# Kernel tuning notes

Measured on AMD Instinct MI355X. Metric: run time of the kernel, lower is better.

Reference implementation:

```python
import jax, jax.numpy as jnp
import numpy as np
import math

E, NNODE = 32768, 2048          # edges, nodes
NUM_SPECIES, EMB = 100, 32
MUL, HIDDEN, N_RBF, LMAX, ENV_P = 16, 256, 8, 3, 6
SL = {0: slice(0, 1), 1: slice(1, 4), 2: slice(4, 9), 3: slice(9, 16)}  # SH blocks


def _cg(j1, m1, j2, m2, j3, m3):
    """Clebsch-Gordan coefficient (Racah formula), complex SH basis."""
    if m1 + m2 != m3:
        return 0.0
    f = math.factorial
    pre = math.sqrt((2*j3+1) * f(j1+j2-j3) * f(j1-j2+j3) * f(-j1+j2+j3) / f(j1+j2+j3+1))
    pre *= math.sqrt(f(j3+m3)*f(j3-m3)*f(j1-m1)*f(j1+m1)*f(j2-m2)*f(j2+m2))
    s = 0.0
    kmin = max(0, j2 - j3 - m1, j1 - j3 + m2)
    kmax = min(j1 + j2 - j3, j1 - m1, j2 + m2)
    for k in range(kmin, kmax + 1):
        s += (-1)**k / (f(k)*f(j1+j2-j3-k)*f(j1-m1-k)*f(j2+m2-k)*f(j3-j2+m1+k)*f(j3-j1-m2+k))
    return pre * s


def _umat(l):
    """Complex->real spherical-harmonics change of basis."""
    U = np.zeros((2*l+1, 2*l+1), dtype=complex)
    U[l, l] = 1.0
    s2 = 1.0 / math.sqrt(2.0)
    for m in range(1, l + 1):
        U[l+m, l-m] = s2
        U[l+m, l+m] = (-1)**m * s2
        U[l-m, l-m] = 1j * s2
        U[l-m, l+m] = -1j * (-1)**m * s2
    return U


def _real_coupling(l1, l2, l3):
    """Real-basis CG coupling tensor, Frobenius-normalized (w3j analogue)."""
    C = np.zeros((2*l1+1, 2*l2+1, 2*l3+1), dtype=complex)
    for a, m1 in enumerate(range(-l1, l1+1)):
        for b, m2 in enumerate(range(-l2, l2+1)):
            for c, m3 in enumerate(range(-l3, l3+1)):
                C[a, b, c] = _cg(l1, m1, l2, m2, l3, m3)
    T = np.einsum('am,bn,ck,mnk->abc', _umat(l1), _umat(l2), _umat(l3).conj(), C)
    Tr, Ti = np.real(T), np.imag(T)
    T = Tr if np.linalg.norm(Tr) >= np.linalg.norm(Ti) else Ti
    n = np.linalg.norm(T)
    return None if n < 1e-8 else (T / n).astype(np.float32)


PATHS = {l3: [] for l3 in range(LMAX + 1)}
for _l1 in range(LMAX + 1):
    for _l2 in range(LMAX + 1):
        for _l3 in range(abs(_l1 - _l2), min(_l1 + _l2, LMAX) + 1):
            _T = _real_coupling(_l1, _l2, _l3)
            if _T is not None:
                PATHS[_l3].append((_l1, _l2, jnp.asarray(_T)))
NPATH = {l3: len(PATHS[l3]) for l3 in range(LMAX + 1)}


def envelope(d):  # polynomial smoothing envelope, p=6, cutoff=1
    p = ENV_P
    e = 1.0 - 0.5*(p+1)*(p+2)*d**p + p*(p+2)*d**(p+1) - 0.5*p*(p+1)*d**(p+2)
    return jnp.where(d < 1.0, e, 0.0)


def bessel(d):  # radial Bessel basis [E] -> [E, N_RBF]
    n = jnp.arange(1, N_RBF + 1, dtype=d.dtype)
    ds = jnp.where(d == 0.0, 1.0, d)[:, None]
    return (math.sqrt(2.0) * jnp.sin(n * jnp.pi * ds) / ds) * envelope(d)[:, None]


def sph_harm16(u):  # real SH l=0..3, component norm (|Y_l|^2 = 2l+1), [E,16]
    x, y, z = u[:, 0], u[:, 1], u[:, 2]
    x2, y2, z2 = x*x, y*y, z*z
    s3, s15, s5 = math.sqrt(3.0), math.sqrt(15.0), math.sqrt(5.0)
    s358, s105 = math.sqrt(35.0/8.0), math.sqrt(105.0)
    s218, s7 = math.sqrt(21.0/8.0), math.sqrt(7.0)
    return jnp.stack([
        jnp.ones_like(x),
        s3*y, s3*z, s3*x,
        s15*x*y, s15*y*z, 0.5*s5*(3*z2 - 1), s15*x*z, 0.5*s15*(x2 - y2),
        s358*y*(3*x2 - y2), s105*x*y*z, s218*y*(5*z2 - 1), 0.5*s7*(5*z2 - 3)*z,
        s218*x*(5*z2 - 1), 0.5*s105*(x2 - y2)*z, s358*x*(x2 - y2),
    ], axis=1)


def dense(x, W):  # e3nn-style bias-free linear, 1/sqrt(fan_in)
    return (x @ W) / math.sqrt(W.shape[0])


def dense_axis(V, W):  # [E,C,K] x [C,D] -> [E,D,K]
    return jnp.einsum('eck,cd->edk', V, W) / math.sqrt(W.shape[0])


def tensor_product(A, B, lmax_out):
    """CG tensor product [E,MUL,16] x [E,MUL,16] -> {l3: [E,MUL*npath,2l3+1]}."""
    out = {}
    for l3 in range(lmax_out + 1):
        scale = math.sqrt(2*l3 + 1)
        parts = [scale * jnp.einsum('ijk,emi,emj->emk', T, A[:, :, SL[l1]], B[:, :, SL[l2]])
                 for (l1, l2, T) in PATHS[l3]]
        out[l3] = jnp.concatenate(parts, axis=1)
    return out


def allegro_layer(x, V, Y, senders, eps, env, alpha, Ww, Wl, Wv):
    w = dense(x, Ww)                                          # [E,MUL]
    node = jax.ops.segment_sum(w[:, :, None] * Y[:, None, :], senders, num_segments=NNODE)
    wY = node[senders] * eps                                  # scatter_sum + map_back
    lmax_out = LMAX if Wv is not None else 0
    tp = tensor_product(wY, V, lmax_out)
    xc = jnp.concatenate([x, tp[0][:, :, 0]], axis=1)         # fold 0e into scalars
    h = jax.nn.silu(dense(xc, Wl[0]))
    h = jax.nn.silu(dense(h, Wl[1]))
    y = env[:, None] * dense(h, Wl[2])
    a2 = alpha**2
    x = (x + a2 * y) / (1.0 + a2)
    if Wv is None:
        return x, None
    Vn = jnp.concatenate(
        [jnp.zeros((V.shape[0], MUL, 1), x.dtype)] +           # no 0e in output irreps
        [dense_axis(tp[l], Wv[l - 1]) for l in (1, 2, 3)], axis=2)
    return x, Vn


def _forward(vectors, varepsilon, alpha, emb, W_tb1, W_tb2, W_tb3, W_tb4,
             W_w0, W_w1, W_l11, W_l12, W_l13, W_v1, W_v2, W_v3,
             W_w2, W_l21, W_l22, W_l23, W_h, W_out,
             senders, receivers, species):
    d = jnp.linalg.norm(vectors, axis=1)
    u = vectors / jnp.where(d == 0.0, 1.0, d)[:, None]
    env = envelope(d)
    eps = 1.0 / jnp.sqrt(1.0 + varepsilon**2)
    x = jnp.concatenate([bessel(d), emb[species[senders]], emb[species[receivers]]], axis=1)
    x = jnp.where(d[:, None] == 0.0, 0.0, x)
    x = jax.nn.silu(dense(x, W_tb1))
    x = jax.nn.silu(dense(x, W_tb2))
    x = jax.nn.silu(dense(x, W_tb3))
    x = dense(x, W_tb4)
    x = env[:, None] * x                                      # [E,HIDDEN]
    Y = sph_harm16(u)                                         # [E,16]
    V = dense(x, W_w0)[:, :, None] * Y[:, None, :]            # [E,MUL,16]
    x, V = allegro_layer(x, V, Y, senders, eps, env, alpha,
                         W_w1, (W_l11, W_l12, W_l13), (W_v1, W_v2, W_v3))
    x, _ = allegro_layer(x, V, Y, senders, eps, env, alpha,
                         W_w2, (W_l21, W_l22, W_l23), None)
    x = dense(x, W_h)
    return env[:, None] * dense(x, W_out)                     # [E,1]


def setup_inputs():
    key = jax.random.key(0)
    ks = jax.random.split(key, 32)
    dirs = jax.random.normal(ks[0], (E, 3), dtype=jnp.float32)
    dirs = dirs / jnp.linalg.norm(dirs, axis=1, keepdims=True)
    r = jax.random.uniform(ks[1], (E, 1), minval=0.05, maxval=0.95, dtype=jnp.float32)
    w = lambda k, s: jax.random.normal(k, s, dtype=jnp.float32)
    n0 = NPATH[0]
    return {
        "vectors": dirs * r,
        "varepsilon": jnp.asarray(4.0, jnp.float32),   # sqrt(avg_num_neighbors=16)
        "alpha": jnp.asarray(1.0, jnp.float32),
        "emb": w(ks[5], (NUM_SPECIES, EMB)),
        "W_tb1": w(ks[6], (N_RBF + 2*EMB, HIDDEN // 8)),
        "W_tb2": w(ks[7], (HIDDEN // 8, HIDDEN // 4)),
        "W_tb3": w(ks[8], (HIDDEN // 4, HIDDEN // 2)),
        "W_tb4": w(ks[9], (HIDDEN // 2, HIDDEN)),
        "W_w0": w(ks[10], (HIDDEN, MUL)),
        "W_w1": w(ks[11], (HIDDEN, MUL)),
        "W_l11": w(ks[12], (HIDDEN + MUL * n0, HIDDEN)),
        "W_l12": w(ks[13], (HIDDEN, HIDDEN)),
        "W_l13": w(ks[14], (HIDDEN, HIDDEN)),
        "W_v1": w(ks[15], (MUL * NPATH[1], MUL)),
        "W_v2": w(ks[16], (MUL * NPATH[2], MUL)),
        "W_v3": w(ks[17], (MUL * NPATH[3], MUL)),
        "W_w2": w(ks[18], (HIDDEN, MUL)),
        "W_l21": w(ks[19], (HIDDEN + MUL * n0, HIDDEN)),
        "W_l22": w(ks[20], (HIDDEN, HIDDEN)),
        "W_l23": w(ks[21], (HIDDEN, HIDDEN)),
        "W_h": w(ks[22], (HIDDEN, 128)),
        "W_out": w(ks[23], (128, 1)),
        "senders": jax.random.randint(ks[2], (E,), 0, NNODE),
        "receivers": jax.random.randint(ks[3], (E,), 0, NNODE),
        "species": jax.random.randint(ks[4], (NNODE,), 0, NUM_SPECIES),
    }


def reference(vectors, varepsilon, alpha, emb, W_tb1, W_tb2, W_tb3, W_tb4,
              W_w0, W_w1, W_l11, W_l12, W_l13, W_v1, W_v2, W_v3,
              W_w2, W_l21, W_l22, W_l23, W_h, W_out,
              senders, receivers, species):
    return _forward(vectors, varepsilon, alpha, emb, W_tb1, W_tb2, W_tb3, W_tb4,
                    W_w0, W_w1, W_l11, W_l12, W_l13, W_v1, W_v2, W_v3,
                    W_w2, W_l21, W_l22, W_l23, W_h, W_out,
                    senders, receivers, species)
```

## Files before the change

kernel.cpp:

```cpp
#include <hip/hip_runtime.h>
#include <cmath>
#include <complex>
#include <cstdio>
#include <cstring>
#include <algorithm>

#define E_EDGES 32768
#define NNODES  2048
#define VN_E    128

namespace cgt {

static double fct(int n){
  static const double f[13] = {1.,1.,2.,6.,24.,120.,720.,5040.,40320.,362880.,
                               3628800.,39916800.,479001600.};
  return f[n];
}

static double cg(int j1,int m1,int j2,int m2,int j3,int m3){
  if (m1+m2 != m3) return 0.0;
  double pre = std::sqrt((2*j3+1)*fct(j1+j2-j3)*fct(j1-j2+j3)*fct(-j1+j2+j3)/fct(j1+j2+j3+1));
  pre *= std::sqrt(fct(j3+m3)*fct(j3-m3)*fct(j1-m1)*fct(j1+m1)*fct(j2-m2)*fct(j2+m2));
  int kmin = 0;
  if (j2-j3-m1 > kmin) kmin = j2-j3-m1;
  if (j1-j3+m2 > kmin) kmin = j1-j3+m2;
  int kmax = j1+j2-j3;
  if (j1-m1 < kmax) kmax = j1-m1;
  if (j2+m2 < kmax) kmax = j2+m2;
  double s = 0.0;
  for (int k=kmin;k<=kmax;k++){
    double d = fct(k)*fct(j1+j2-j3-k)*fct(j1-m1-k)*fct(j2+m2-k)*fct(j3-j2+m1+k)*fct(j3-j1-m2+k);
    s += ((k&1)? -1.0:1.0)/d;
  }
  return pre*s;
}

typedef std::complex<double> cd;

static void umat(int l, cd U[7][7]){
  for (int a=0;a<7;a++) for (int b=0;b<7;b++) U[a][b]=cd(0,0);
  U[l][l] = cd(1,0);
  double s2 = 1.0/std::sqrt(2.0);
  for (int m=1;m<=l;m++){
    double sg = (m&1)? -1.0 : 1.0;
    U[l+m][l-m] = cd(s2,0);
    U[l+m][l+m] = cd(sg*s2,0);
    U[l-m][l-m] = cd(0, s2);
    U[l-m][l+m] = cd(0, -sg*s2);
  }
}

static bool realCoupling(int l1,int l2,int l3, double T[7][7][7]){
  cd U1[7][7],U2[7][7],U3[7][7];
  umat(l1,U1); umat(l2,U2); umat(l3,U3);
  int n1=2*l1+1, n2=2*l2+1, n3=2*l3+1;
  double Cg[7][7][7];
  for (int m=0;m<n1;m++) for(int n=0;n<n2;n++) for(int k=0;k<n3;k++)
    Cg[m][n][k] = cg(l1,m-l1,l2,n-l2,l3,k-l3);
  double Tr[7][7][7], Ti[7][7][7];
  double nr=0, ni=0;
  for (int a=0;a<n1;a++) for(int b=0;b<n2;b++) for(int c=0;c<n3;c++){
    cd s(0,0);
    for (int m=0;m<n1;m++){
      if (U1[a][m]==cd(0,0)) continue;
      for (int n=0;n<n2;n++){
        if (U2[b][n]==cd(0,0)) continue;
        for (int k=0;k<n3;k++){
          double cgv = Cg[m][n][k];
          if (cgv==0.0) continue;
          s += U1[a][m]*U2[b][n]*std::conj(U3[c][k])*cgv;
        }
      }
    }
    Tr[a][b][c]=s.real(); Ti[a][b][c]=s.imag();
    nr += s.real()*s.real(); ni += s.imag()*s.imag();
  }
  bool useR = (nr >= ni);
  double nn = std::sqrt(useR? nr : ni);
  if (nn < 1e-8) return false;
  for (int a=0;a<n1;a++)for(int b=0;b<n2;b++)for(int c=0;c<n3;c++)
    T[a][b][c] = (useR? Tr[a][b][c] : Ti[a][b][c])/nn;
  return true;
}

struct Tables {
  float val[4096];
  int   ij[4096];
  int   pmeta[40*4];
  int   ccnt[40*8];
  int   l3base[4];
  int   l3np[4];
  int   npaths;
  int   nent;
  int   tptot;
  int   pairs[256];
  float TD[256*30*8];
  int   sl_origc[40];
  int   npairs;
};

struct PathTmp {
  int l1,l2,l3, tpoff, kd;
  int ec;
  double T[7][7][7];
};

static void build(Tables& tb){
  static PathTmp paths[40];
  int np = 0, tpoff = 0;
  int l3start[5];
  for (int l3=0;l3<=3;l3++){
    tb.l3base[l3] = tpoff;
    l3start[l3] = np;
    int kd = 2*l3+1;
    for (int l1=0;l1<=3;l1++) for (int l2=0;l2<=3;l2++){
      int lo = (l1>l2)? l1-l2 : l2-l1;
      int hi = std::min(l1+l2,3);
      if (l3 < lo || l3 > hi) continue;
      PathTmp& pt = paths[np];
      if (!realCoupling(l1,l2,l3,pt.T)) continue;
      pt.l1=l1; pt.l2=l2; pt.l3=l3; pt.kd=kd; pt.tpoff=tpoff;
      double scale = std::sqrt((double)kd);
      int cnt = 0;
      for (int a=0;a<2*l1+1;a++)for(int b=0;b<2*l2+1;b++)for(int c=0;c<kd;c++)
        if (std::fabs(pt.T[a][b][c]*scale) > 1e-7) cnt++;
      pt.ec = cnt;
      tpoff += 16*kd;
      np++;
    }
  }
  l3start[4] = np;
  for (int l3=0;l3<=3;l3++) tb.l3np[l3] = l3start[l3+1]-l3start[l3];
  static int order[40];
  for (int i=0;i<np;i++) order[i]=i;
  for (int l3=0;l3<=3;l3++)
    std::sort(order+l3start[l3], order+l3start[l3+1],
              [&](int a,int b){ return paths[a].ec > paths[b].ec; });
  std::memset(tb.TD, 0, sizeof(tb.TD));
  std::memset(tb.pairs, 0, sizeof(tb.pairs));
  static int pmap[16][16];
  for (int i=0;i<16;i++) for (int j=0;j<16;j++) pmap[i][j] = -1;
  int npr = 0;
  int ep = 0;
  for (int slot=0; slot<np; slot++){
    const PathTmp& pt = paths[order[slot]];
    double scale = std::sqrt((double)pt.kd);
    int s1 = pt.l1*pt.l1, s2 = pt.l2*pt.l2;
    tb.pmeta[slot*4+0] = pt.tpoff;
    tb.pmeta[slot*4+1] = ep;
    tb.sl_origc[slot] = ((pt.tpoff - tb.l3base[pt.l3]) / (16*pt.kd)) * 16;
    int tot = 0;
    for (int c=0;c<pt.kd;c++){
      int cnt = 0;
      for (int a=0;a<2*pt.l1+1;a++)for(int b=0;b<2*pt.l2+1;b++){
        double v = pt.T[a][b][c]*scale;
        if (std::fabs(v) > 1e-7){
          tb.val[ep] = (float)v;
          tb.ij[ep]  = (s1+a) | ((s2+b)<<8);
          ep++; cnt++;
          if (pt.l3 >= 1){
            int aa = s1+a, bb = s2+b;
            int pi = pmap[aa][bb];
            if (pi < 0){ pi = npr; pmap[aa][bb] = pi;
                         tb.pairs[npr] = aa | (bb<<8); npr++; }
            tb.TD[(pi*30 + (slot-4))*8 + c] = (float)v;
          }
        }
      }
      tb.ccnt[slot*8+c] = cnt;
      tot += cnt;
    }
    for (int c=pt.kd;c<8;c++) tb.ccnt[slot*8+c]=0;
    tb.pmeta[slot*4+2] = tot;
    tb.pmeta[slot*4+3] = pt.kd;
  }
  if (npr & 1){ tb.pairs[npr] = 0; npr++; }
  tb.npairs = npr;
  tb.npaths = np; tb.nent = ep; tb.tptot = tpoff;
}

}


enum GFlags { F_NONE=0, F_SILU=1, F_ENV=2, F_RESID=4 };

typedef _Float16 half8 __attribute__((ext_vector_type(8)));
typedef __attribute__((ext_vector_type(4))) float f32x4;

__device__ inline unsigned short f2h(float f){
  union { _Float16 h; unsigned short u; } x;
  x.h = (_Float16)f;
  return x.u;
}
__device__ inline float h2f(unsigned short u){
  union { _Float16 h; unsigned short u; } x; x.u = u;
  return (float)x.h;
}

__device__ inline int swz(int row, int kh){
  int b = row*64 + kh*2;
  return b ^ (((row >> 1) & 3) << 4);
}

template<int FLAGS, int A16>
__global__ __launch_bounds__(256) void mgemm_k(
    const void* __restrict__ A1v, const void* __restrict__ A2v,
    int K1, int K, const unsigned short* __restrict__ Wt, int N,
    unsigned short* Cout, const float* __restrict__ env,
    const float* __restrict__ alphap, const unsigned short* Xres)
{
  __shared__ unsigned short AsB[128*32];
  __shared__ unsigned short BsB[128*32];
  const int tid  = threadIdx.x;
  const int wave = tid >> 6, lane = tid & 63;
  const int bm = blockIdx.x*128, bn = blockIdx.y*128;
  const int wr = (wave >> 1)*64, wc = (wave & 1)*64;
  const int K2 = K - K1;
  f32x4 acc[4][4] = {};

  const int sr  = tid >> 3;
  const int skq = (tid & 7) * 4;
  const int sr2 = tid >> 1;
  const int skh = (tid & 1) * 16;
  const int bn_ = tid >> 1;
  const int bkh = (tid & 1) * 16;

  for (int k0 = 0; k0 < K; k0 += 32) {
    if (A16) {
      int kk = k0 + skh;
      const unsigned short* ap = (kk < K1)
        ? (const unsigned short*)A1v + (size_t)(bm + sr2)*K1 + kk
        : (const unsigned short*)A2v + (size_t)(bm + sr2)*K2 + (kk - K1);
      uint4 u0 = *(const uint4*)ap;
      uint4 u1 = *(const uint4*)(ap + 8);
      *(uint4*)((char*)AsB + swz(sr2, skh))     = u0;
      *(uint4*)((char*)AsB + swz(sr2, skh + 8)) = u1;
    } else {
#pragma unroll
      for (int q = 0; q < 4; q++) {
        int row = q*32 + sr;
        int grow = bm + row;
        int kk = k0 + skq;
        float4 f4 = (kk < K1)
          ? *(const float4*)((const float*)A1v + (size_t)grow*K1 + kk)
          : *(const float4*)((const float*)A2v + (size_t)grow*K2 + (kk - K1));
        ushort4 u;
        u.x = f2h(f4.x); u.y = f2h(f4.y); u.z = f2h(f4.z); u.w = f2h(f4.w);
        *(ushort4*)((char*)AsB + swz(row, skq)) = u;
      }
    }
    {
      const unsigned short* s = Wt + (size_t)(bn + bn_)*K + k0 + bkh;
#pragma unroll
      for (int q = 0; q < 4; q++) {
        ushort4 u = *(const ushort4*)(s + q*4);
        *(ushort4*)((char*)BsB + swz(bn_, bkh + q*4)) = u;
      }
    }
    __syncthreads();
    const int fr = lane & 15, fk = (lane >> 4) * 8;
    half8 af[4], bf[4];
#pragma unroll
    for (int i = 0; i < 4; i++)
      af[i] = *(half8*)((char*)AsB + swz(wr + i*16 + fr, fk));
#pragma unroll
    for (int j = 0; j < 4; j++)
      bf[j] = *(half8*)((char*)BsB + swz(wc + j*16 + fr, fk));
#pragma unroll
    for (int i = 0; i < 4; i++)
#pragma unroll
      for (int j = 0; j < 4; j++)
        acc[i][j] = __builtin_amdgcn_mfma_f32_16x16x32_f16(af[i], bf[j], acc[i][j], 0, 0, 0);
    __syncthreads();
  }

  const float rscale = 1.f/sqrtf((float)K);
  float a2 = 0.f, inv1a2 = 1.f;
  if (FLAGS & F_RESID) { float al = alphap[0]; a2 = al*al; inv1a2 = 1.f/(1.f+a2); }
#pragma unroll
  for (int i = 0; i < 4; i++) {
#pragma unroll
    for (int r = 0; r < 4; r++) {
      int row = bm + wr + i*16 + ((lane >> 4) << 2) + r;
      float ev = (FLAGS & F_ENV) ? env[row] : 1.f;
#pragma unroll
      for (int j = 0; j < 4; j++) {
        int col = bn + wc + j*16 + (lane & 15);
        float v = acc[i][j][r]*rscale;
        if (FLAGS & F_SILU) v = v/(1.f+__expf(-v));
        if (FLAGS & F_ENV)  v *= ev;
        if (FLAGS & F_RESID) v = (h2f(Xres[(size_t)row*N+col]) + a2*v)*inv1a2;
        Cout[(size_t)row*N+col] = f2h(v);
      }
    }
  }
}

__global__ __launch_bounds__(256) void mlp3_k(
    const unsigned short* __restrict__ X, const unsigned short* __restrict__ T0,
    const unsigned short* __restrict__ W1t, const unsigned short* __restrict__ W2t,
    const unsigned short* __restrict__ W3t, unsigned short* __restrict__ Out,
    const float* __restrict__ env, const float* __restrict__ alphap)
{
  __shared__ unsigned short AsB[64*32];
  __shared__ unsigned short BsB[256*32];
  __shared__ unsigned short Hs[64*264];
  const int tid  = threadIdx.x;
  const int wave = tid >> 6, lane = tid & 63;
  const int bm = blockIdx.x*64;
  const int wc = wave*64;
  const int fr = lane & 15, fk = (lane >> 4) * 8;
  const int r4 = (lane >> 4) << 2;
  const int sra = tid >> 2;
  const int ska = (tid & 3) * 8;
  const int srb = tid >> 1;
  const int skb = (tid & 1) * 16;
  f32x4 acc[4][4] = {};

  for (int k0 = 0; k0 < 320; k0 += 32) {
    {
      int kk = k0 + ska;
      const unsigned short* ap = (kk < 256)
        ? X  + (size_t)(bm + sra)*256 + kk
        : T0 + (size_t)(bm + sra)*64  + (kk - 256);
      uint4 u = *(const uint4*)ap;
      *(uint4*)((char*)AsB + swz(sra, ska)) = u;
    }
#pragma unroll
    for (int h = 0; h < 2; h++) {
      int n = h*128 + srb;
      const unsigned short* s = W1t + (size_t)n*320 + k0 + skb;
      uint4 u0 = *(const uint4*)s;
      uint4 u1 = *(const uint4*)(s + 8);
      *(uint4*)((char*)BsB + swz(n, skb))     = u0;
      *(uint4*)((char*)BsB + swz(n, skb + 8)) = u1;
    }
    __syncthreads();
    half8 af[4], bf[4];
#pragma unroll
    for (int i = 0; i < 4; i++)
      af[i] = *(half8*)((char*)AsB + swz(i*16 + fr, fk));
#pragma unroll
    for (int j = 0; j < 4; j++)
      bf[j] = *(half8*)((char*)BsB + swz(wc + j*16 + fr, fk));
#pragma unroll
    for (int i = 0; i < 4; i++)
#pragma unroll
      for (int j = 0; j < 4; j++)
        acc[i][j] = __builtin_amdgcn_mfma_f32_16x16x32_f16(af[i], bf[j], acc[i][j], 0, 0, 0);
    __syncthreads();
  }
  const float rs320 = 0.055901699437494740f;
#pragma unroll
  for (int i = 0; i < 4; i++)
#pragma unroll
    for (int r = 0; r < 4; r++) {
      int row = i*16 + r4 + r;
#pragma unroll
      for (int j = 0; j < 4; j++) {
        int col = wc + j*16 + fr;
        float v = acc[i][j][r]*rs320;
        v = v/(1.f+__expf(-v));
        Hs[row*264 + col] = f2h(v);
        acc[i][j][r] = 0.f;
      }
    }
  __syncthreads();

  for (int k0 = 0; k0 < 256; k0 += 32) {
#pragma unroll
    for (int h = 0; h < 2; h++) {
      int n = h*128 + srb;
      const unsigned short* s = W2t + (size_t)n*256 + k0 + skb;
      uint4 u0 = *(const uint4*)s;
      uint4 u1 = *(const uint4*)(s + 8);
      *(uint4*)((char*)BsB + swz(n, skb))     = u0;
      *(uint4*)((char*)BsB + swz(n, skb + 8)) = u1;
    }
    __syncthreads();
    half8 af[4], bf[4];
#pragma unroll
    for (int i = 0; i < 4; i++)
      af[i] = *(half8*)(Hs + (i*16 + fr)*264 + k0 + fk);
#pragma unroll
    for (int j = 0; j < 4; j++)
      bf[j] = *(half8*)((char*)BsB + swz(wc + j*16 + fr, fk));
#pragma unroll
    for (int i = 0; i < 4; i++)
#pragma unroll
      for (int j = 0; j < 4; j++)
        acc[i][j] = __builtin_amdgcn_mfma_f32_16x16x32_f16(af[i], bf[j], acc[i][j], 0, 0, 0);
    __syncthreads();
  }
#pragma unroll
  for (int i = 0; i < 4; i++)
#pragma unroll
    for (int r = 0; r < 4; r++) {
      int row = i*16 + r4 + r;
#pragma unroll
      for (int j = 0; j < 4; j++) {
        int col = wc + j*16 + fr;
        float v = acc[i][j][r]*0.0625f;
        v = v/(1.f+__expf(-v));
        Hs[row*264 + col] = f2h(v);
        acc[i][j][r] = 0.f;
      }
    }
  __syncthreads();

  for (int k0 = 0; k0 < 256; k0 += 32) {
#pragma unroll
    for (int h = 0; h < 2; h++) {
      int n = h*128 + srb;
      const unsigned short* s = W3t + (size_t)n*256 + k0 + skb;
      uint4 u0 = *(const uint4*)s;
      uint4 u1 = *(const uint4*)(s + 8);
      *(uint4*)((char*)BsB + swz(n, skb))     = u0;
      *(uint4*)((char*)BsB + swz(n, skb + 8)) = u1;
    }
    __syncthreads();
    half8 af[4], bf[4];
#pragma unroll
    for (int i = 0; i < 4; i++)
      af[i] = *(half8*)(Hs + (i*16 + fr)*264 + k0 + fk);
#pragma unroll
    for (int j = 0; j < 4; j++)
      bf[j] = *(half8*)((char*)BsB + swz(wc + j*16 + fr, fk));
#pragma unroll
    for (int i = 0; i < 4; i++)
#pragma unroll
      for (int j = 0; j < 4; j++)
        acc[i][j] = __builtin_amdgcn_mfma_f32_16x16x32_f16(af[i], bf[j], acc[i][j], 0, 0, 0);
    __syncthreads();
  }
  float al = alphap[0];
  float a2 = al*al, inv1a2 = 1.f/(1.f+a2);
#pragma unroll
  for (int i = 0; i < 4; i++)
#pragma unroll
    for (int r = 0; r < 4; r++) {
      int row = bm + i*16 + r4 + r;
      float ev = env[row];
#pragma unroll
      for (int j = 0; j < 4; j++) {
        int col = wc + j*16 + fr;
        float v = acc[i][j][r]*0.0625f*ev;
        v = (h2f(X[(size_t)row*256+col]) + a2*v)*inv1a2;
        Out[(size_t)row*256+col] = f2h(v);
      }
    }
}

__global__ __launch_bounds__(512) void vn_k(
    const float* __restrict__ node, const unsigned short* __restrict__ V,
    const int* __restrict__ senders, const float* __restrict__ varepsp,
    const int* __restrict__ pairsG, const unsigned short* __restrict__ Gtt,
    unsigned short* __restrict__ Vn, int Kdim,
    const int* __restrict__ pmeta, const int* __restrict__ entIJ,
    const float* __restrict__ entVal, unsigned short* __restrict__ tp0)
{
  __shared__ unsigned short Ab[VN_E*264];
  __shared__ unsigned short Bb[VN_E*264];
  __shared__ int Ps[256];
  const int tid = threadIdx.x;
  const int e0 = blockIdx.x * VN_E;
  const int wave = tid >> 6, lane = tid & 63;
  float ve = varepsp[0];
  float eps = rsqrtf(1.f + ve*ve);
  if (tid < 256) Ps[tid] = pairsG[tid];
#pragma unroll
  for (int rr = 0; rr < 16; rr++) {
    int row = wave*16 + rr;
    int s = senders[e0 + row];
    float4 fa = *(const float4*)(node + ((size_t)s << 8) + 4*lane);
    uint2 ub = *(const uint2*)(V + (((size_t)(e0 + row)) << 8) + 4*lane);
    unsigned short* ad = Ab + row*264 + 4*lane;
    unsigned short* bd = Bb + row*264 + 4*lane;
    uint2 ua;
    ua.x = (unsigned)f2h(fa.x*eps) | ((unsigned)f2h(fa.y*eps) << 16);
    ua.y = (unsigned)f2h(fa.z*eps) | ((unsigned)f2h(fa.w*eps) << 16);
    *(uint2*)ad = ua;
    *(uint2*)bd = ub;
  }
  __syncthreads();
  for (int o = tid; o < VN_E*64; o += 512) {
    int e = o >> 6, c = o & 63;
    int p = c >> 4, m = c & 15;
    const unsigned short* Ae = Ab + e*264;
    const unsigned short* Be = Bb + e*264;
    int es = pmeta[p*4+1], ec = pmeta[p*4+2];
    float acc = 0.f;
    for (int t = 0; t < ec; t++) {
      int ij = entIJ[es+t];
      acc += entVal[es+t] * h2f(Ae[((ij&255)<<4)+m]) * h2f(Be[(((ij>>8)&255)<<4)+m]);
    }
    tp0[((size_t)(e0+e)<<6) + pmeta[p*4+0] + m] = f2h(acc);
  }
  const int rowb = (wave & 1) * 64;
  const int wc   = (wave >> 1) * 64;
  const int fr = lane & 15, fk = (lane >> 4) * 8;
  const int pairSel = fk >> 4;
  const int moff = fk & 15;
  const int nslab = Kdim >> 5;
  f32x4 acc[4][4] = {};

  const unsigned short* Ar0 = Ab + (rowb + fr)*264;
  const unsigned short* Br0 = Bb + (rowb + fr)*264;
  const unsigned short* Ar1 = Ab + (rowb + 16 + fr)*264;
  const unsigned short* Br1 = Bb + (rowb + 16 + fr)*264;
  const unsigned short* Ar2 = Ab + (rowb + 32 + fr)*264;
  const unsigned short* Br2 = Bb + (rowb + 32 + fr)*264;
  const unsigned short* Ar3 = Ab + (rowb + 48 + fr)*264;
  const unsigned short* Br3 = Bb + (rowb + 48 + fr)*264;

  const unsigned short* gp = Gtt + ((size_t)(wc + fr)) * 32 + fk;
  half8 b0 = *(const half8*)(gp);
  half8 b1 = *(const half8*)(gp + 512);
  half8 b2 = *(const half8*)(gp + 1024);
  half8 b3 = *(const half8*)(gp + 1536);
  half8 c0 = b0, c1 = b1, c2 = b2, c3 = b3;
  if (nslab > 1) {
    const unsigned short* g1 = gp + 8192;
    c0 = *(const half8*)(g1);
    c1 = *(const half8*)(g1 + 512);
    c2 = *(const half8*)(g1 + 1024);
    c3 = *(const half8*)(g1 + 1536);
  }
  int p0 = Ps[pairSel];
  int aoff = ((p0 & 255) << 4) + moff;
  int boff = (((p0 >> 8) & 255) << 4) + moff;
  half8 rA0 = *(const half8*)(Ar0 + aoff);
  half8 rB0 = *(const half8*)(Br0 + boff);
  half8 rA1 = *(const half8*)(Ar1 + aoff);
  half8 rB1 = *(const half8*)(Br1 + boff);
  half8 rA2 = *(const half8*)(Ar2 + aoff);
  half8 rB2 = *(const half8*)(Br2 + boff);
  half8 rA3 = *(const half8*)(Ar3 + aoff);
  half8 rB3 = *(const half8*)(Br3 + boff);

  for (int sl = 0; sl < nslab; sl++) {
    half8 a0 = rA0 * rB0;
    half8 a1 = rA1 * rB1;
    half8 a2 = rA2 * rB2;
    half8 a3 = rA3 * rB3;
    if (sl + 1 < nslab) {
      int pn = Ps[2*(sl + 1) + pairSel];
      int aoffn = ((pn & 255) << 4) + moff;
      int boffn = (((pn >> 8) & 255) << 4) + moff;
      rA0 = *(const half8*)(Ar0 + aoffn);
      rB0 = *(const half8*)(Br0 + boffn);
      rA1 = *(const half8*)(Ar1 + aoffn);
      rB1 = *(const half8*)(Br1 + boffn);
      rA2 = *(const half8*)(Ar2 + aoffn);
      rB2 = *(const half8*)(Br2 + boffn);
      rA3 = *(const half8*)(Ar3 + aoffn);
      rB3 = *(const half8*)(Br3 + boffn);
    }
    half8 d0, d1, d2, d3;
    if (sl + 2 < nslab) {
      const unsigned short* gn = gp + (size_t)(sl + 2) * 8192;
      d0 = *(const half8*)(gn);
      d1 = *(const half8*)(gn + 512);
      d2 = *(const half8*)(gn + 1024);
      d3 = *(const half8*)(gn + 1536);
    } else { d0 = c0; d1 = c1; d2 = c2; d3 = c3; }
    acc[0][0] = __builtin_amdgcn_mfma_f32_16x16x32_f16(a0, b0, acc[0][0], 0, 0, 0);
    acc[1][0] = __builtin_amdgcn_mfma_f32_16x16x32_f16(a1, b0, acc[1][0], 0, 0, 0);
    acc[2][0] = __builtin_amdgcn_mfma_f32_16x16x32_f16(a2, b0, acc[2][0], 0, 0, 0);
    acc[3][0] = __builtin_amdgcn_mfma_f32_16x16x32_f16(a3, b0, acc[3][0], 0, 0, 0);
    acc[0][1] = __builtin_amdgcn_mfma_f32_16x16x32_f16(a0, b1, acc[0][1], 0, 0, 0);
    acc[1][1] = __builtin_amdgcn_mfma_f32_16x16x32_f16(a1, b1, acc[1][1], 0, 0, 0);
    acc[2][1] = __builtin_amdgcn_mfma_f32_16x16x32_f16(a2, b1, acc[2][1], 0, 0, 0);
    acc[3][1] = __builtin_amdgcn_mfma_f32_16x16x32_f16(a3, b1, acc[3][1], 0, 0, 0);
    acc[0][2] = __builtin_amdgcn_mfma_f32_16x16x32_f16(a0, b2, acc[0][2], 0, 0, 0);
    acc[1][2] = __builtin_amdgcn_mfma_f32_16x16x32_f16(a1, b2, acc[1][2], 0, 0, 0);
    acc[2][2] = __builtin_amdgcn_mfma_f32_16x16x32_f16(a2, b2, acc[2][2], 0, 0, 0);
    acc[3][2] = __builtin_amdgcn_mfma_f32_16x16x32_f16(a3, b2, acc[3][2], 0, 0, 0);
    acc[0][3] = __builtin_amdgcn_mfma_f32_16x16x32_f16(a0, b3, acc[0][3], 0, 0, 0);
    acc[1][3] = __builtin_amdgcn_mfma_f32_16x16x32_f16(a1, b3, acc[1][3], 0, 0, 0);
    acc[2][3] = __builtin_amdgcn_mfma_f32_16x16x32_f16(a2, b3, acc[2][3], 0, 0, 0);
    acc[3][3] = __builtin_amdgcn_mfma_f32_16x16x32_f16(a3, b3, acc[3][3], 0, 0, 0);
    b0 = c0; b1 = c1; b2 = c2; b3 = c3;
    c0 = d0; c1 = d1; c2 = d2; c3 = d3;
  }
  const int r4 = (lane >> 4) << 2;
#pragma unroll
  for (int rg = 0; rg < 4; rg++) {
#pragma unroll
    for (int j = 0; j < 4; j++) {
#pragma unroll
      for (int r = 0; r < 4; r++) {
        int row = e0 + rowb + rg*16 + r4 + r;
        int col = wc + j*16 + fr;
        Vn[(size_t)row*256 + col] = f2h(acc[rg][j][r]);
      }
    }
  }
}

__global__ void gbuild_k(const float* __restrict__ TD,
    const float* __restrict__ Wv1, const float* __restrict__ Wv2,
    const float* __restrict__ Wv3, const int* __restrict__ sl_origc,
    unsigned short* __restrict__ Gt, int Kdim, int npairs,
    int s1b, int s1e, int s2e, int s3e)
{
  int k = blockIdx.x*256 + threadIdx.x;
  if (k >= Kdim) return;
  int col = blockIdx.y;
  int pair = k >> 4, m = k & 15;
  int d = col & 15, kabs = col >> 4;
  float acc = 0.f;
  if (kabs > 0 && pair < npairs) {
    const float* Wv; int ss, se, kloc;
    if (kabs < 4)      { Wv = Wv1; ss = s1b; se = s1e; kloc = kabs - 1; }
    else if (kabs < 9) { Wv = Wv2; ss = s1e; se = s2e; kloc = kabs - 4; }
    else               { Wv = Wv3; ss = s2e; se = s3e; kloc = kabs - 9; }
    for (int slot = ss; slot < se; slot++)
      acc += TD[((pair*30) + (slot - 4))*8 + kloc] * Wv[(sl_origc[slot] + m)*16 + d];
    acc *= rsqrtf((float)(16*(se - ss)));
  }
  Gt[((size_t)((k >> 5)*256 + col))*32 + (k & 31)] = f2h(acc);
}

struct WDesc { const float* src; unsigned short* dst; int K; int lgN; };
struct WPack { WDesc d[8]; };
__global__ void wcvt_k(WPack p){
  WDesc d = p.d[blockIdx.y];
  int total = d.K << d.lgN;
  int gid = blockIdx.x*256 + threadIdx.x;
  if (gid >= total) return;
  int k = gid >> d.lgN, n = gid & ((1 << d.lgN) - 1);
  d.dst[(size_t)n*d.K + k] = f2h(d.src[gid]);
}

__global__ void whc_k(const float* __restrict__ Wh, const float* __restrict__ Wout,
                      float* __restrict__ hc)
{
  int k = threadIdx.x;
  float s = 0.f;
#pragma unroll 16
  for (int j = 0; j < 128; j++) s += Wh[k*128 + j] * Wout[j];
  hc[k] = s;
}

__global__ void final256_k(const unsigned short* __restrict__ X,
    const float* __restrict__ hc, const float* __restrict__ env,
    float* __restrict__ out)
{
  const int e = blockIdx.x*256 + threadIdx.x;
  float acc = 0.f;
#pragma unroll 16
  for (int k = 0; k < 256; k++) acc += h2f(X[((size_t)e<<8)+k])*hc[k];
  out[e] = env[e]*acc*0.0055242717280199023f;
}

template<int FLAGS>
__global__ __launch_bounds__(256) void gemm_k(
    const float* __restrict__ A1, const float* __restrict__ A2,
    int K1, int K, const float* __restrict__ W, int N,
    float* Cout,
    const float* __restrict__ env, const float* __restrict__ alphap,
    const float* Xres)
{
  __shared__ float As[16][68];
  __shared__ float Ws[16][68];
  const int tid = threadIdx.x;
  const int bm = blockIdx.x * 64;
  const int bn = blockIdx.y * 64;
  const int tx = tid & 15, ty = tid >> 4;
  const int K2 = K - K1;
  float acc[4][4] = {};
  for (int k0 = 0; k0 < K; k0 += 16) {
#pragma unroll
    for (int i = 0; i < 4; i++) {
      int idx = tid + i*256;
      int m = idx >> 4, kk = idx & 15;
      int k = k0 + kk;
      float v = 0.f;
      if (k < K) {
        int row = bm + m;
        v = (k < K1) ? A1[(size_t)row*K1 + k] : A2[(size_t)row*K2 + (k-K1)];
      }
      As[kk][m] = v;
    }
#pragma unroll
    for (int i = 0; i < 4; i++) {
      int idx = tid + i*256;
      int n = idx & 63, kk = idx >> 6;
      int k = k0 + kk, col = bn + n;
      Ws[kk][n] = (k < K && col < N) ? W[(size_t)k*N + col] : 0.f;
    }
    __syncthreads();
#pragma unroll
    for (int kk = 0; kk < 16; kk++) {
      float a[4], b[4];
#pragma unroll
      for (int i=0;i<4;i++) a[i] = As[kk][ty*4+i];
#pragma unroll
      for (int j=0;j<4;j++) b[j] = Ws[kk][tx*4+j];
#pragma unroll
      for (int i=0;i<4;i++)
#pragma unroll
        for (int j=0;j<4;j++)
          acc[i][j] += a[i]*b[j];
    }
    __syncthreads();
  }
  const float rscale = 1.f/sqrtf((float)K);
  float a2 = 0.f, inv1a2 = 1.f;
  if (FLAGS & F_RESID) { float al = alphap[0]; a2 = al*al; inv1a2 = 1.f/(1.f+a2); }
#pragma unroll
  for (int i=0;i<4;i++) {
    int row = bm + ty*4 + i;
    float ev = (FLAGS & F_ENV) ? env[row] : 1.f;
#pragma unroll
    for (int j=0;j<4;j++) {
      int col = bn + tx*4 + j;
      if (col >= N) continue;
      float v = acc[i][j]*rscale;
      if (FLAGS & F_SILU) v = v/(1.f+__expf(-v));
      if (FLAGS & F_ENV)  v *= ev;
      if (FLAGS & F_RESID) v = (Xres[(size_t)row*N+col] + a2*v)*inv1a2;
      Cout[(size_t)row*N+col] = v;
    }
  }
}

__global__ __launch_bounds__(256) void dense16_k(const unsigned short* __restrict__ A,
    const float* __restrict__ W, float* __restrict__ C)
{
  __shared__ float As[16*256];
  const int r0 = blockIdx.x << 4;
  const int tid = threadIdx.x;
  for (int i = tid; i < 16*256; i += 256)
    As[i] = h2f(A[((size_t)r0<<8) + i]);
  __syncthreads();
  const int r = tid >> 4, n = tid & 15;
  float acc = 0.f;
#pragma unroll 8
  for (int k = 0; k < 256; k++)
    acc += As[(r<<8)+k] * W[(k<<4)+n];
  C[((size_t)(r0+r)<<4)+n] = acc * 0.0625f;
}

__global__ __launch_bounds__(256) void dense16v_k(const unsigned short* __restrict__ A,
    const float* __restrict__ W0, const float* __restrict__ W1,
    const float* __restrict__ Y, unsigned short* __restrict__ V,
    float* __restrict__ wb)
{
  __shared__ float As[16*256];
  __shared__ float w0s[256];
  const int r0 = blockIdx.x << 4;
  const int tid = threadIdx.x;
  for (int i = tid; i < 16*256; i += 256)
    As[i] = h2f(A[((size_t)r0<<8) + i]);
  __syncthreads();
  const int r = tid >> 4, n = tid & 15;
  float a0 = 0.f, a1 = 0.f;
#pragma unroll 8
  for (int k = 0; k < 256; k++) {
    float xv = As[(r<<8)+k];
    a0 += xv * W0[(k<<4)+n];
    a1 += xv * W1[(k<<4)+n];
  }
  w0s[tid] = a0 * 0.0625f;
  wb[((size_t)(r0+r)<<4)+n] = a1 * 0.0625f;
  __syncthreads();
  for (int i = tid; i < 4096; i += 256) {
    int e = i >> 8, idx = i & 255;
    V[(((size_t)(r0+e))<<8) + idx] = f2h(w0s[(e<<4)+(idx&15)] * Y[((r0+e)<<4)+(idx>>4)]);
  }
}

__global__ void edge_init_k(const float* __restrict__ vectors, const int* __restrict__ senders,
    const int* __restrict__ receivers, const int* __restrict__ species,
    const float* __restrict__ emb, float* __restrict__ envb, float* __restrict__ Yb,
    float* __restrict__ x72)
{
  const int e = blockIdx.x*256 + threadIdx.x;
  float vx = vectors[e*3+0], vy = vectors[e*3+1], vz = vectors[e*3+2];
  float d = sqrtf(vx*vx+vy*vy+vz*vz);
  float dd = (d==0.f) ? 1.f : d;
  float invd = 1.f/dd;
  float x = vx*invd, y = vy*invd, z = vz*invd;
  float d2=d*d, d3=d2*d, d6=d3*d3, d7=d6*d, d8=d7*d;
  float envv = (d<1.f) ? (1.f - 28.f*d6 + 48.f*d7 - 21.f*d8) : 0.f;
  envb[e] = envv;
  float mask = (d==0.f)?0.f:1.f;
  const float SQ2 = 1.41421356237309515f;
  const float PIf = 3.14159265358979323846f;
  float* xr = x72 + (size_t)e*72;
#pragma unroll
  for (int n=1;n<=8;n++)
    xr[n-1] = SQ2 * sinf((float)n*PIf*dd)*invd*envv*mask;
  int sp_s = species[senders[e]], sp_r = species[receivers[e]];
  const float* es_ = emb + (size_t)sp_s*32;
  const float* er_ = emb + (size_t)sp_r*32;
#pragma unroll 8
  for (int k=0;k<32;k++){ xr[8+k] = es_[k]*mask; xr[40+k] = er_[k]*mask; }
  float x2=x*x, y2=y*y, z2=z*z;
  const float s3=1.7320508075688772f, s15=3.872983346207417f, s5=2.23606797749979f;
  const float s358=2.0916500663351889f, s105=10.246950765959598f;
  const float s218=1.6201851746019651f, s7=2.6457513110645907f;
  float* Yr = Yb + ((size_t)e<<4);
  Yr[0]=1.f;           Yr[1]=s3*y;          Yr[2]=s3*z;           Yr[3]=s3*x;
  Yr[4]=s15*x*y;       Yr[5]=s15*y*z;       Yr[6]=0.5f*s5*(3.f*z2-1.f);
  Yr[7]=s15*x*z;       Yr[8]=0.5f*s15*(x2-y2);
  Yr[9]=s358*y*(3.f*x2-y2);  Yr[10]=s105*x*y*z;  Yr[11]=s218*y*(5.f*z2-1.f);
  Yr[12]=0.5f*s7*(5.f*z2-3.f)*z;  Yr[13]=s218*x*(5.f*z2-1.f);
  Yr[14]=0.5f*s105*(x2-y2)*z;     Yr[15]=s358*x*(x2-y2);
}

__global__ void hist_k(const int* __restrict__ senders, int* cnt){
  int e = blockIdx.x*256 + threadIdx.x;
  atomicAdd(&cnt[senders[e]], 1);
}

__global__ void scan_k(const int* __restrict__ cnt, int* __restrict__ starts,
                       int* __restrict__ cursor){
  __shared__ int s[NNODES];
  const int tid = threadIdx.x;
  for (int i = tid; i < NNODES; i += 256) s[i] = cnt[i];
  __syncthreads();
  if (tid == 0) {
    int run = 0;
    for (int i = 0; i < NNODES; i++) { int c = s[i]; s[i] = run; run += c; }
  }
  __syncthreads();
  for (int i = tid; i < NNODES; i += 256) { starts[i] = s[i]; cursor[i] = s[i]; }
  if (tid == 0) starts[NNODES] = E_EDGES;
}

__global__ void perm_k(const int* __restrict__ senders, int* cursor,
                       int* __restrict__ perm){
  int e = blockIdx.x*256 + threadIdx.x;
  int pos = atomicAdd(&cursor[senders[e]], 1);
  perm[pos] = e;
}

__global__ __launch_bounds__(256) void nodesum_k(const float* __restrict__ w,
    const float* __restrict__ Y, const int* __restrict__ perm,
    const int* __restrict__ starts, float* __restrict__ node)
{
  __shared__ float buf[8*32];
  const int n = blockIdx.x;
  const int tid = threadIdx.x;
  const int s0 = starts[n], s1 = starts[n+1];
  const int a = tid >> 4, m = tid & 15;
  float acc = 0.f;
  for (int i = s0; i < s1; i += 8) {
    int nb = s1 - i; if (nb > 8) nb = 8;
    int slot = tid >> 5, comp = tid & 31;
    if (slot < nb) {
      int e = perm[i + slot];
      buf[slot*32 + comp] = (comp < 16) ? w[(e<<4)+comp] : Y[(e<<4)+comp-16];
    }
    __syncthreads();
    for (int q = 0; q < nb; q++)
      acc += buf[q*32 + m] * buf[q*32 + 16 + a];
    __syncthreads();
  }
  node[((size_t)n<<8) + tid] = acc;
}

__global__ void tp2_k(const float* __restrict__ node, const unsigned short* __restrict__ Vn,
    const int* __restrict__ senders, const float* __restrict__ varepsp,
    const int* __restrict__ pmeta, const int* __restrict__ entIJ,
    const float* __restrict__ entVal, unsigned short* __restrict__ tp0)
{
  const int gid = blockIdx.x*256 + threadIdx.x;
  const int e = gid >> 6, c = gid & 63;
  const int p = c >> 4, m = c & 15;
  float ve = varepsp[0];
  float eps = rsqrtf(1.f + ve*ve);
  int s = senders[e];
  const float* Am = &node[((size_t)s<<8)];
  const unsigned short* Bm = &Vn[((size_t)e<<8)];
  int es = pmeta[p*4+1], ec = pmeta[p*4+2];
  float acc = 0.f;
  for (int t=0;t<ec;t++){
    int ij = entIJ[es+t];
    acc += entVal[es+t] * Am[((ij&255)<<4) + m] * h2f(Bm[(((ij>>8)&255)<<4) + m]);
  }
  tp0[((size_t)e<<6) + pmeta[p*4+0] + m] = f2h(acc * eps);
}


static void launch_gemm(int flags, const float* A1, const float* A2, int K1, int K,
    const float* W, int N, float* C, const float* env, const float* alphap,
    const float* Xres, hipStream_t stream)
{
  dim3 grid(E_EDGES/64, (N+63)/64);
  switch(flags){
    case F_SILU:        gemm_k<F_SILU>       <<<grid,256,0,stream>>>(A1,A2,K1,K,W,N,C,env,alphap,Xres); break;
    case F_ENV:         gemm_k<F_ENV>        <<<grid,256,0,stream>>>(A1,A2,K1,K,W,N,C,env,alphap,Xres); break;
    default: break;
  }
}

static void launch_mgemm(int flags, int a16, const void* A1, const void* A2, int K1, int K,
    const unsigned short* Wt, int N, unsigned short* C, const float* env,
    const float* alphap, const unsigned short* Xres, hipStream_t stream)
{
  dim3 grid(E_EDGES/128, N/128);
  if (a16) {
    switch(flags){
      case F_ENV:         mgemm_k<F_ENV,1>        <<<grid,256,0,stream>>>(A1,A2,K1,K,Wt,N,C,env,alphap,Xres); break;
      default: break;
    }
  } else {
    switch(flags){
      case F_SILU:        mgemm_k<F_SILU,0>       <<<grid,256,0,stream>>>(A1,A2,K1,K,Wt,N,C,env,alphap,Xres); break;
      default: break;
    }
  }
}

extern "C" void kernel_launch(void* const* d_in, const int* in_sizes, int n_in,
                              void* d_out, int out_size, void* d_ws, size_t ws_size,
                              hipStream_t stream)
{
  const float* vectors = (const float*)d_in[0];
  const float* vareps  = (const float*)d_in[1];
  const float* alpha   = (const float*)d_in[2];
  const float* emb     = (const float*)d_in[3];
  const float* W_tb1   = (const float*)d_in[4];
  const float* W_tb2   = (const float*)d_in[5];
  const float* W_tb3   = (const float*)d_in[6];
  const float* W_tb4   = (const float*)d_in[7];
  const float* W_w0    = (const float*)d_in[8];
  const float* W_w1    = (const float*)d_in[9];
  const float* W_l11   = (const float*)d_in[10];
  const float* W_l12   = (const float*)d_in[11];
  const float* W_l13   = (const float*)d_in[12];
  const float* W_v1    = (const float*)d_in[13];
  const float* W_v2    = (const float*)d_in[14];
  const float* W_v3    = (const float*)d_in[15];
  const float* W_w2    = (const float*)d_in[16];
  const float* W_l21   = (const float*)d_in[17];
  const float* W_l22   = (const float*)d_in[18];
  const float* W_l23   = (const float*)d_in[19];
  const float* W_h     = (const float*)d_in[20];
  const float* W_out   = (const float*)d_in[21];
  const int* senders   = (const int*)d_in[22];
  const int* receivers = (const int*)d_in[23];
  const int* species   = (const int*)d_in[24];

  static cgt::Tables tb;
  cgt::build(tb);
  const int Kdim = tb.npairs * 16;

  char* ws = (char*)d_ws;
  size_t off = 0;
  auto alloc = [&](size_t bytes)->void*{
    void* p = ws + off; off += (bytes + 255) & ~(size_t)255; return p;
  };
  float* t_val = (float*)alloc(sizeof(tb.val));
  int*   t_ij  = (int*)  alloc(sizeof(tb.ij));
  int*   t_pm  = (int*)  alloc(sizeof(tb.pmeta));
  float* t_td  = (float*)alloc(sizeof(tb.TD));
  int*   t_pr  = (int*)  alloc(sizeof(tb.pairs));
  int*   t_oc  = (int*)  alloc(sizeof(tb.sl_origc));
  float* envb  = (float*)alloc((size_t)E_EDGES*4);
  float* Yb    = (float*)alloc((size_t)E_EDGES*16*4);
  float* xb    = (float*)alloc((size_t)E_EDGES*256*4);
  float* Vb    = (float*)alloc((size_t)E_EDGES*256*4);
  float* bufA  = (float*)alloc((size_t)E_EDGES*256*4);
  float* bufB  = (float*)alloc((size_t)E_EDGES*256*4);
  float* wb    = (float*)alloc((size_t)E_EDGES*16*4);
  float* tp0b  = (float*)alloc((size_t)E_EDGES*64*4);
  float* nodeb = (float*)alloc((size_t)NNODES*256*4);
  float* hcb   = (float*)alloc(256*4);
  int* cntb    = (int*)alloc(NNODES*4);
  int* startsb = (int*)alloc((NNODES+1)*4);
  int* cursorb = (int*)alloc(NNODES*4);
  int* permb   = (int*)alloc(E_EDGES*4);
  unsigned short* Gt = (unsigned short*)alloc((size_t)256*Kdim*2);
  unsigned short* Wt_tb3 = (unsigned short*)alloc(64*128*2);
  unsigned short* Wt_tb4 = (unsigned short*)alloc(128*256*2);
  unsigned short* Wt_l11 = (unsigned short*)alloc(320*256*2);
  unsigned short* Wt_l12 = (unsigned short*)alloc(256*256*2);
  unsigned short* Wt_l13 = (unsigned short*)alloc(256*256*2);
  unsigned short* Wt_l21 = (unsigned short*)alloc(320*256*2);
  unsigned short* Wt_l22 = (unsigned short*)alloc(256*256*2);
  unsigned short* Wt_l23 = (unsigned short*)alloc(256*256*2);
  if (off > ws_size) {
    fprintf(stderr, "[allegro] workspace too small: need %zu, have %zu\n", off, ws_size);
    return;
  }
  unsigned short* xb16 = (unsigned short*)xb;
  unsigned short* bB16 = (unsigned short*)bufB;
  unsigned short* tp016 = (unsigned short*)tp0b;
  unsigned short* V16 = (unsigned short*)Vb;

  hipMemcpyAsync(t_val, tb.val,     sizeof(tb.val),     hipMemcpyHostToDevice, stream);
  hipMemcpyAsync(t_ij,  tb.ij,      sizeof(tb.ij),      hipMemcpyHostToDevice, stream);
  hipMemcpyAsync(t_pm,  tb.pmeta,   sizeof(tb.pmeta),   hipMemcpyHostToDevice, stream);
  hipMemcpyAsync(t_td,  tb.TD,      sizeof(tb.TD),      hipMemcpyHostToDevice, stream);
  hipMemcpyAsync(t_pr,  tb.pairs,   sizeof(tb.pairs),   hipMemcpyHostToDevice, stream);
  hipMemcpyAsync(t_oc,  tb.sl_origc,sizeof(tb.sl_origc),hipMemcpyHostToDevice, stream);

  const int s1b = tb.l3np[0];
  const int s1e = s1b + tb.l3np[1];
  const int s2e = s1e + tb.l3np[2];
  const int s3e = s2e + tb.l3np[3];

  {
    dim3 g((Kdim + 255)/256, 256);
    gbuild_k<<<g, 256, 0, stream>>>(t_td, W_v1, W_v2, W_v3, t_oc, Gt, Kdim,
                                    tb.npairs, s1b, s1e, s2e, s3e);
  }
  {
    WPack p;
    p.d[0] = { W_tb3, Wt_tb3,  64, 7 };
    p.d[1] = { W_tb4, Wt_tb4, 128, 8 };
    p.d[2] = { W_l11, Wt_l11, 320, 8 };
    p.d[3] = { W_l12, Wt_l12, 256, 8 };
    p.d[4] = { W_l13, Wt_l13, 256, 8 };
    p.d[5] = { W_l21, Wt_l21, 320, 8 };
    p.d[6] = { W_l22, Wt_l22, 256, 8 };
    p.d[7] = { W_l23, Wt_l23, 256, 8 };
    dim3 g(320, 8);
    wcvt_k<<<g, 256, 0, stream>>>(p);
  }
  whc_k<<<1, 256, 0, stream>>>(W_h, W_out, hcb);

  hipMemsetAsync(cntb, 0, NNODES*4, stream);
  hist_k<<<E_EDGES/256, 256, 0, stream>>>(senders, cntb);
  scan_k<<<1, 256, 0, stream>>>(cntb, startsb, cursorb);
  perm_k<<<E_EDGES/256, 256, 0, stream>>>(senders, cursorb, permb);

  edge_init_k<<<E_EDGES/256, 256, 0, stream>>>(vectors, senders, receivers, species,
                                               emb, envb, Yb, bufA);
  launch_gemm (F_SILU, bufA, nullptr, 72, 72,  W_tb1, 32,  bufB, envb, alpha, nullptr, stream);
  launch_gemm (F_SILU, bufB, nullptr, 32, 32,  W_tb2, 64,  bufA, envb, alpha, nullptr, stream);
  launch_mgemm(F_SILU, 0, bufA, nullptr, 64, 64,  Wt_tb3, 128, bB16, envb, alpha, nullptr, stream);
  launch_mgemm(F_ENV,  1, bB16, nullptr, 128,128, Wt_tb4, 256, xb16, envb, alpha, nullptr, stream);
  dense16v_k<<<E_EDGES/16, 256, 0, stream>>>(xb16, W_w0, W_w1, Yb, V16, wb);

  nodesum_k<<<NNODES, 256, 0, stream>>>(wb, Yb, permb, startsb, nodeb);
  vn_k<<<E_EDGES/VN_E, 512, 0, stream>>>(nodeb, V16, senders, vareps, t_pr, Gt,
                                         V16, Kdim, t_pm, t_ij, t_val, tp016);
  mlp3_k<<<E_EDGES/64, 256, 0, stream>>>(xb16, tp016, Wt_l11, Wt_l12, Wt_l13,
                                         xb16, envb, alpha);

  dense16_k<<<E_EDGES/16, 256, 0, stream>>>(xb16, W_w2, wb);
  nodesum_k<<<NNODES, 256, 0, stream>>>(wb, Yb, permb, startsb, nodeb);
  tp2_k<<<E_EDGES*64/256, 256, 0, stream>>>(nodeb, V16, senders, vareps, t_pm, t_ij,
                                            t_val, tp016);
  mlp3_k<<<E_EDGES/64, 256, 0, stream>>>(xb16, tp016, Wt_l21, Wt_l22, Wt_l23,
                                         xb16, envb, alpha);

  final256_k<<<E_EDGES/256, 256, 0, stream>>>(xb16, hcb, envb, (float*)d_out);
}
```

Measured before the change: 436.6 us.

## Fuse two-body MLP and w0/w1 projection into one MFMA kernel

Replaces the chain of five launches (two fp32 SIMT GEMMs, two MFMA GEMMs, and the dense16v projection) with a single per-64-edge kernel. The kernel runs all four two-body layers plus the combined W_w0/W_w1 projection on fp16 MFMA, keeps intermediate activations in LDS, and writes only the final features, V and w. This removes the global round trips of the intermediates and several launches, and moves the first two layers from fp32 FMA to fp16 MFMA. The cost is a large LDS footprint, low MFMA tile utilization on the small layers, extra weight-conversion launches, and fp16 rounding of the first-layer inputs and weights.

```diff
diff --git a/kernel.cpp b/kernel.cpp
--- a/kernel.cpp
+++ b/kernel.cpp
@@ -182,8 +182,6 @@
 }
 
 
-enum GFlags { F_NONE=0, F_SILU=1, F_ENV=2, F_RESID=4 };
-
 typedef _Float16 half8 __attribute__((ext_vector_type(8)));
 typedef __attribute__((ext_vector_type(4))) float f32x4;
 
@@ -202,97 +200,203 @@
   return b ^ (((row >> 1) & 3) << 4);
 }
 
-template<int FLAGS, int A16>
-__global__ __launch_bounds__(256) void mgemm_k(
-    const void* __restrict__ A1v, const void* __restrict__ A2v,
-    int K1, int K, const unsigned short* __restrict__ Wt, int N,
-    unsigned short* Cout, const float* __restrict__ env,
-    const float* __restrict__ alphap, const unsigned short* Xres)
+__device__ inline float silu(float v){ return v/(1.f+__expf(-v)); }
+
+#define MFMA16 __builtin_amdgcn_mfma_f32_16x16x32_f16
+
+__global__ __launch_bounds__(256) void tb_fused_k(
+    const float* __restrict__ X72, const unsigned short* __restrict__ Wt1,
+    const unsigned short* __restrict__ Wt2, const unsigned short* __restrict__ Wt3,
+    const unsigned short* __restrict__ Wt4, const unsigned short* __restrict__ Wt01,
+    const float* __restrict__ Yb, const float* __restrict__ envb,
+    unsigned short* __restrict__ Xout, unsigned short* __restrict__ V,
+    float* __restrict__ wb)
 {
-  __shared__ unsigned short AsB[128*32];
-  __shared__ unsigned short BsB[128*32];
+  __shared__ unsigned short AsB[64*32];
+  __shared__ unsigned short BsB[256*32];
+  __shared__ unsigned short HsA[64*264];
+  __shared__ unsigned short HsB[64*264];
+  __shared__ float w0s[64*16];
   const int tid  = threadIdx.x;
   const int wave = tid >> 6, lane = tid & 63;
-  const int bm = blockIdx.x*128, bn = blockIdx.y*128;
-  const int wr = (wave >> 1)*64, wc = (wave & 1)*64;
-  const int K2 = K - K1;
-  f32x4 acc[4][4] = {};
-
-  const int sr  = tid >> 3;
-  const int skq = (tid & 7) * 4;
-  const int sr2 = tid >> 1;
-  const int skh = (tid & 1) * 16;
-  const int bn_ = tid >> 1;
-  const int bkh = (tid & 1) * 16;
-
-  for (int k0 = 0; k0 < K; k0 += 32) {
-    if (A16) {
-      int kk = k0 + skh;
-      const unsigned short* ap = (kk < K1)
-        ? (const unsigned short*)A1v + (size_t)(bm + sr2)*K1 + kk
-        : (const unsigned short*)A2v + (size_t)(bm + sr2)*K2 + (kk - K1);
-      uint4 u0 = *(const uint4*)ap;
-      uint4 u1 = *(const uint4*)(ap + 8);
-      *(uint4*)((char*)AsB + swz(sr2, skh))     = u0;
-      *(uint4*)((char*)AsB + swz(sr2, skh + 8)) = u1;
-    } else {
-#pragma unroll
-      for (int q = 0; q < 4; q++) {
-        int row = q*32 + sr;
-        int grow = bm + row;
-        int kk = k0 + skq;
-        float4 f4 = (kk < K1)
-          ? *(const float4*)((const float*)A1v + (size_t)grow*K1 + kk)
-          : *(const float4*)((const float*)A2v + (size_t)grow*K2 + (kk - K1));
-        ushort4 u;
-        u.x = f2h(f4.x); u.y = f2h(f4.y); u.z = f2h(f4.z); u.w = f2h(f4.w);
-        *(ushort4*)((char*)AsB + swz(row, skq)) = u;
-      }
-    }
-    {
-      const unsigned short* s = Wt + (size_t)(bn + bn_)*K + k0 + bkh;
-#pragma unroll
-      for (int q = 0; q < 4; q++) {
-        ushort4 u = *(const ushort4*)(s + q*4);
-        *(ushort4*)((char*)BsB + swz(bn_, bkh + q*4)) = u;
-      }
-    }
-    __syncthreads();
-    const int fr = lane & 15, fk = (lane >> 4) * 8;
-    half8 af[4], bf[4];
-#pragma unroll
-    for (int i = 0; i < 4; i++)
-      af[i] = *(half8*)((char*)AsB + swz(wr + i*16 + fr, fk));
+  const int bm = blockIdx.x*64;
+  const int mrow = wave*16;
+  const int fr = lane & 15, fk = (lane >> 4) * 8;
+  const int r4 = (lane >> 4) << 2;
+  const int sra = tid >> 2, ska = (tid & 3) * 8;
+  const int srb = tid >> 1, skb = (tid & 1) * 16;
+
+  {
+    f32x4 acc[2] = {};
+    for (int k0 = 0; k0 < 96; k0 += 32) {
+      {
+        unsigned short u[8];
+        int rowg = bm + sra;
+#pragma unroll
+        for (int q = 0; q < 8; q++) {
+          int k = k0 + ska + q;
+          u[q] = (k < 72) ? f2h(X72[(size_t)rowg*72 + k]) : (unsigned short)0;
+        }
+        *(ushort4*)((char*)AsB + swz(sra, ska))     = *(ushort4*)&u[0];
+        *(ushort4*)((char*)AsB + swz(sra, ska + 4)) = *(ushort4*)&u[4];
+      }
+      if (tid < 64) {
+        int n = tid >> 1, kb = (tid & 1) * 16;
+        unsigned short u[16];
+#pragma unroll
+        for (int q = 0; q < 16; q++) {
+          int k = k0 + kb + q;
+          u[q] = (k < 72) ? Wt1[n*72 + k] : (unsigned short)0;
+        }
+        *(uint4*)((char*)BsB + swz(n, kb))     = *(uint4*)&u[0];
+        *(uint4*)((char*)BsB + swz(n, kb + 8)) = *(uint4*)&u[8];
+      }
+      __syncthreads();
+      half8 af = *(half8*)((char*)AsB + swz(mrow + fr, fk));
+      half8 b0 = *(half8*)((char*)BsB + swz(fr, fk));
+      half8 b1 = *(half8*)((char*)BsB + swz(16 + fr, fk));
+      acc[0] = MFMA16(af, b0, acc[0], 0, 0, 0);
+      acc[1] = MFMA16(af, b1, acc[1], 0, 0, 0);
+      __syncthreads();
+    }
+    const float rs = 0.11785113019775793f;
+#pragma unroll
+    for (int j = 0; j < 2; j++)
+#pragma unroll
+      for (int r = 0; r < 4; r++) {
+        int row = mrow + r4 + r;
+        HsA[row*264 + j*16 + fr] = f2h(silu(acc[j][r]*rs));
+      }
+    __syncthreads();
+  }
+
+  {
+    f32x4 acc[4] = {};
+    if (tid < 128) {
+      int n = tid >> 1, kb = (tid & 1) * 16;
+      const unsigned short* s = Wt2 + n*32 + kb;
+      uint4 u0 = *(const uint4*)s;
+      uint4 u1 = *(const uint4*)(s + 8);
+      *(uint4*)((char*)BsB + swz(n, kb))     = u0;
+      *(uint4*)((char*)BsB + swz(n, kb + 8)) = u1;
+    }
+    __syncthreads();
+    half8 af = *(half8*)(HsA + (mrow + fr)*264 + fk);
+#pragma unroll
+    for (int j = 0; j < 4; j++) {
+      half8 bf = *(half8*)((char*)BsB + swz(j*16 + fr, fk));
+      acc[j] = MFMA16(af, bf, acc[j], 0, 0, 0);
+    }
+    __syncthreads();
+    const float rs = 0.17677669529663687f;
 #pragma unroll
     for (int j = 0; j < 4; j++)
-      bf[j] = *(half8*)((char*)BsB + swz(wc + j*16 + fr, fk));
-#pragma unroll
-    for (int i = 0; i < 4; i++)
-#pragma unroll
-      for (int j = 0; j < 4; j++)
-        acc[i][j] = __builtin_amdgcn_mfma_f32_16x16x32_f16(af[i], bf[j], acc[i][j], 0, 0, 0);
-    __syncthreads();
-  }
-
-  const float rscale = 1.f/sqrtf((float)K);
-  float a2 = 0.f, inv1a2 = 1.f;
-  if (FLAGS & F_RESID) { float al = alphap[0]; a2 = al*al; inv1a2 = 1.f/(1.f+a2); }
-#pragma unroll
-  for (int i = 0; i < 4; i++) {
+#pragma unroll
+      for (int r = 0; r < 4; r++) {
+        int row = mrow + r4 + r;
+        HsB[row*264 + j*16 + fr] = f2h(silu(acc[j][r]*rs));
+      }
+    __syncthreads();
+  }
+
+  {
+    f32x4 acc[8] = {};
+    for (int k0 = 0; k0 < 64; k0 += 32) {
+      {
+        int n = srb, kb = skb;
+        const unsigned short* s = Wt3 + n*64 + k0 + kb;
+        uint4 u0 = *(const uint4*)s;
+        uint4 u1 = *(const uint4*)(s + 8);
+        *(uint4*)((char*)BsB + swz(n, kb))     = u0;
+        *(uint4*)((char*)BsB + swz(n, kb + 8)) = u1;
+      }
+      __syncthreads();
+      half8 af = *(half8*)(HsB + (mrow + fr)*264 + k0 + fk);
+#pragma unroll
+      for (int j = 0; j < 8; j++) {
+        half8 bf = *(half8*)((char*)BsB + swz(j*16 + fr, fk));
+        acc[j] = MFMA16(af, bf, acc[j], 0, 0, 0);
+      }
+      __syncthreads();
+    }
+    const float rs = 0.125f;
+#pragma unroll
+    for (int j = 0; j < 8; j++)
+#pragma unroll
+      for (int r = 0; r < 4; r++) {
+        int row = mrow + r4 + r;
+        HsA[row*264 + j*16 + fr] = f2h(silu(acc[j][r]*rs));
+      }
+    __syncthreads();
+  }
+
+  {
+    f32x4 acc[16] = {};
+    for (int k0 = 0; k0 < 128; k0 += 32) {
+#pragma unroll
+      for (int h = 0; h < 2; h++) {
+        int n = h*128 + srb;
+        const unsigned short* s = Wt4 + (size_t)n*128 + k0 + skb;
+        uint4 u0 = *(const uint4*)s;
+        uint4 u1 = *(const uint4*)(s + 8);
+        *(uint4*)((char*)BsB + swz(n, skb))     = u0;
+        *(uint4*)((char*)BsB + swz(n, skb + 8)) = u1;
+      }
+      __syncthreads();
+      half8 af = *(half8*)(HsA + (mrow + fr)*264 + k0 + fk);
+#pragma unroll
+      for (int j = 0; j < 16; j++) {
+        half8 bf = *(half8*)((char*)BsB + swz(j*16 + fr, fk));
+        acc[j] = MFMA16(af, bf, acc[j], 0, 0, 0);
+      }
+      __syncthreads();
+    }
+    const float rs = 0.08838834764831845f;
+#pragma unroll
+    for (int j = 0; j < 16; j++)
+#pragma unroll
+      for (int r = 0; r < 4; r++) {
+        int row = mrow + r4 + r;
+        float v = acc[j][r]*rs*envb[bm + row];
+        unsigned short hv = f2h(v);
+        HsB[row*264 + j*16 + fr] = hv;
+        Xout[((size_t)(bm + row))*256 + j*16 + fr] = hv;
+      }
+    __syncthreads();
+  }
+
+  {
+    f32x4 acc[2] = {};
+    for (int k0 = 0; k0 < 256; k0 += 32) {
+      if (tid < 64) {
+        int n = tid >> 1, kb = (tid & 1) * 16;
+        const unsigned short* s = Wt01 + (size_t)n*256 + k0 + kb;
+        uint4 u0 = *(const uint4*)s;
+        uint4 u1 = *(const uint4*)(s + 8);
+        *(uint4*)((char*)BsB + swz(n, kb))     = u0;
+        *(uint4*)((char*)BsB + swz(n, kb + 8)) = u1;
+      }
+      __syncthreads();
+      half8 af = *(half8*)(HsB + (mrow + fr)*264 + k0 + fk);
+      half8 b0 = *(half8*)((char*)BsB + swz(fr, fk));
+      half8 b1 = *(half8*)((char*)BsB + swz(16 + fr, fk));
+      acc[0] = MFMA16(af, b0, acc[0], 0, 0, 0);
+      acc[1] = MFMA16(af, b1, acc[1], 0, 0, 0);
+      __syncthreads();
+    }
 #pragma unroll
     for (int r = 0; r < 4; r++) {
-      int row = bm + wr + i*16 + ((lane >> 4) << 2) + r;
-      float ev = (FLAGS & F_ENV) ? env[row] : 1.f;
-#pragma unroll
-      for (int j = 0; j < 4; j++) {
-        int col = bn + wc + j*16 + (lane & 15);
-        float v = acc[i][j][r]*rscale;
-        if (FLAGS & F_SILU) v = v/(1.f+__expf(-v));
-        if (FLAGS & F_ENV)  v *= ev;
-        if (FLAGS & F_RESID) v = (h2f(Xres[(size_t)row*N+col]) + a2*v)*inv1a2;
-        Cout[(size_t)row*N+col] = f2h(v);
-      }
-    }
+      int row = mrow + r4 + r;
+      w0s[row*16 + fr] = acc[0][r]*0.0625f;
+      wb[((size_t)(bm + row))*16 + fr] = acc[1][r]*0.0625f;
+    }
+    __syncthreads();
+  }
+
+  for (int i = tid; i < 64*256; i += 256) {
+    int e = i >> 8, idx = i & 255;
+    V[(((size_t)(bm + e)) << 8) + idx] =
+        f2h(w0s[e*16 + (idx & 15)] * Yb[(bm + e)*16 + (idx >> 4)]);
   }
 }
 
@@ -347,7 +451,7 @@
     for (int i = 0; i < 4; i++)
 #pragma unroll
       for (int j = 0; j < 4; j++)
-        acc[i][j] = __builtin_amdgcn_mfma_f32_16x16x32_f16(af[i], bf[j], acc[i][j], 0, 0, 0);
+        acc[i][j] = MFMA16(af[i], bf[j], acc[i][j], 0, 0, 0);
     __syncthreads();
   }
   const float rs320 = 0.055901699437494740f;
@@ -359,9 +463,7 @@
 #pragma unroll
       for (int j = 0; j < 4; j++) {
         int col = wc + j*16 + fr;
-        float v = acc[i][j][r]*rs320;
-        v = v/(1.f+__expf(-v));
-        Hs[row*264 + col] = f2h(v);
+        Hs[row*264 + col] = f2h(silu(acc[i][j][r]*rs320));
         acc[i][j][r] = 0.f;
       }
     }
@@ -389,7 +491,7 @@
     for (int i = 0; i < 4; i++)
 #pragma unroll
       for (int j = 0; j < 4; j++)
-        acc[i][j] = __builtin_amdgcn_mfma_f32_16x16x32_f16(af[i], bf[j], acc[i][j], 0, 0, 0);
+        acc[i][j] = MFMA16(af[i], bf[j], acc[i][j], 0, 0, 0);
     __syncthreads();
   }
 #pragma unroll
@@ -400,9 +502,7 @@
 #pragma unroll
       for (int j = 0; j < 4; j++) {
         int col = wc + j*16 + fr;
-        float v = acc[i][j][r]*0.0625f;
-        v = v/(1.f+__expf(-v));
-        Hs[row*264 + col] = f2h(v);
+        Hs[row*264 + col] = f2h(silu(acc[i][j][r]*0.0625f));
         acc[i][j][r] = 0.f;
       }
     }
@@ -430,7 +530,7 @@
     for (int i = 0; i < 4; i++)
 #pragma unroll
       for (int j = 0; j < 4; j++)
-        acc[i][j] = __builtin_amdgcn_mfma_f32_16x16x32_f16(af[i], bf[j], acc[i][j], 0, 0, 0);
+        acc[i][j] = MFMA16(af[i], bf[j], acc[i][j], 0, 0, 0);
     __syncthreads();
   }
   float al = alphap[0];
@@ -564,22 +664,22 @@
       d2 = *(const half8*)(gn + 1024);
       d3 = *(const half8*)(gn + 1536);
     } else { d0 = c0; d1 = c1; d2 = c2; d3 = c3; }
-    acc[0][0] = __builtin_amdgcn_mfma_f32_16x16x32_f16(a0, b0, acc[0][0], 0, 0, 0);
-    acc[1][0] = __builtin_amdgcn_mfma_f32_16x16x32_f16(a1, b0, acc[1][0], 0, 0, 0);
-    acc[2][0] = __builtin_amdgcn_mfma_f32_16x16x32_f16(a2, b0, acc[2][0], 0, 0, 0);
-    acc[3][0] = __builtin_amdgcn_mfma_f32_16x16x32_f16(a3, b0, acc[3][0], 0, 0, 0);
-    acc[0][1] = __builtin_amdgcn_mfma_f32_16x16x32_f16(a0, b1, acc[0][1], 0, 0, 0);
-    acc[1][1] = __builtin_amdgcn_mfma_f32_16x16x32_f16(a1, b1, acc[1][1], 0, 0, 0);
-    acc[2][1] = __builtin_amdgcn_mfma_f32_16x16x32_f16(a2, b1, acc[2][1], 0, 0, 0);
-    acc[3][1] = __builtin_amdgcn_mfma_f32_16x16x32_f16(a3, b1, acc[3][1], 0, 0, 0);
-    acc[0][2] = __builtin_amdgcn_mfma_f32_16x16x32_f16(a0, b2, acc[0][2], 0, 0, 0);
-    acc[1][2] = __builtin_amdgcn_mfma_f32_16x16x32_f16(a1, b2, acc[1][2], 0, 0, 0);
-    acc[2][2] = __builtin_amdgcn_mfma_f32_16x16x32_f16(a2, b2, acc[2][2], 0, 0, 0);
-    acc[3][2] = __builtin_amdgcn_mfma_f32_16x16x32_f16(a3, b2, acc[3][2], 0, 0, 0);
-    acc[0][3] = __builtin_amdgcn_mfma_f32_16x16x32_f16(a0, b3, acc[0][3], 0, 0, 0);
-    acc[1][3] = __builtin_amdgcn_mfma_f32_16x16x32_f16(a1, b3, acc[1][3], 0, 0, 0);
-    acc[2][3] = __builtin_amdgcn_mfma_f32_16x16x32_f16(a2, b3, acc[2][3], 0, 0, 0);
-    acc[3][3] = __builtin_amdgcn_mfma_f32_16x16x32_f16(a3, b3, acc[3][3], 0, 0, 0);
+    acc[0][0] = MFMA16(a0, b0, acc[0][0], 0, 0, 0);
+    acc[1][0] = MFMA16(a1, b0, acc[1][0], 0, 0, 0);
+    acc[2][0] = MFMA16(a2, b0, acc[2][0], 0, 0, 0);
+    acc[3][0] = MFMA16(a3, b0, acc[3][0], 0, 0, 0);
+    acc[0][1] = MFMA16(a0, b1, acc[0][1], 0, 0, 0);
+    acc[1][1] = MFMA16(a1, b1, acc[1][1], 0, 0, 0);
+    acc[2][1] = MFMA16(a2, b1, acc[2][1], 0, 0, 0);
+    acc[3][1] = MFMA16(a3, b1, acc[3][1], 0, 0, 0);
+    acc[0][2] = MFMA16(a0, b2, acc[0][2], 0, 0, 0);
+    acc[1][2] = MFMA16(a1, b2, acc[1][2], 0, 0, 0);
+    acc[2][2] = MFMA16(a2, b2, acc[2][2], 0, 0, 0);
+    acc[3][2] = MFMA16(a3, b2, acc[3][2], 0, 0, 0);
+    acc[0][3] = MFMA16(a0, b3, acc[0][3], 0, 0, 0);
+    acc[1][3] = MFMA16(a1, b3, acc[1][3], 0, 0, 0);
+    acc[2][3] = MFMA16(a2, b3, acc[2][3], 0, 0, 0);
+    acc[3][3] = MFMA16(a3, b3, acc[3][3], 0, 0, 0);
     b0 = c0; b1 = c1; b2 = c2; b3 = c3;
     c0 = d0; c1 = d1; c2 = d2; c3 = d3;
   }
@@ -623,7 +723,7 @@
 }
 
 struct WDesc { const float* src; unsigned short* dst; int K; int lgN; };
-struct WPack { WDesc d[8]; };
+struct WPack { WDesc d[10]; };
 __global__ void wcvt_k(WPack p){
   WDesc d = p.d[blockIdx.y];
   int total = d.K << d.lgN;
@@ -631,6 +731,14 @@
   if (gid >= total) return;
   int k = gid >> d.lgN, n = gid & ((1 << d.lgN) - 1);
   d.dst[(size_t)n*d.K + k] = f2h(d.src[gid]);
+}
+
+__global__ void wcvt01_k(const float* __restrict__ W0, const float* __restrict__ W1,
+                         unsigned short* __restrict__ dst){
+  int gid = blockIdx.x*256 + threadIdx.x;
+  int k = gid >> 5, n = gid & 31;
+  float v = (n < 16) ? W0[k*16 + n] : W1[k*16 + (n - 16)];
+  dst[(size_t)n*256 + k] = f2h(v);
 }
 
 __global__ void whc_k(const float* __restrict__ Wh, const float* __restrict__ Wout,
@@ -652,78 +760,6 @@
 #pragma unroll 16
   for (int k = 0; k < 256; k++) acc += h2f(X[((size_t)e<<8)+k])*hc[k];
   out[e] = env[e]*acc*0.0055242717280199023f;
-}
-
-template<int FLAGS>
-__global__ __launch_bounds__(256) void gemm_k(
-    const float* __restrict__ A1, const float* __restrict__ A2,
-    int K1, int K, const float* __restrict__ W, int N,
-    float* Cout,
-    const float* __restrict__ env, const float* __restrict__ alphap,
-    const float* Xres)
-{
-  __shared__ float As[16][68];
-  __shared__ float Ws[16][68];
-  const int tid = threadIdx.x;
-  const int bm = blockIdx.x * 64;
-  const int bn = blockIdx.y * 64;
-  const int tx = tid & 15, ty = tid >> 4;
-  const int K2 = K - K1;
-  float acc[4][4] = {};
-  for (int k0 = 0; k0 < K; k0 += 16) {
-#pragma unroll
-    for (int i = 0; i < 4; i++) {
-      int idx = tid + i*256;
-      int m = idx >> 4, kk = idx & 15;
-      int k = k0 + kk;
-      float v = 0.f;
-      if (k < K) {
-        int row = bm + m;
-        v = (k < K1) ? A1[(size_t)row*K1 + k] : A2[(size_t)row*K2 + (k-K1)];
-      }
-      As[kk][m] = v;
-    }
-#pragma unroll
-    for (int i = 0; i < 4; i++) {
-      int idx = tid + i*256;
-      int n = idx & 63, kk = idx >> 6;
-      int k = k0 + kk, col = bn + n;
-      Ws[kk][n] = (k < K && col < N) ? W[(size_t)k*N + col] : 0.f;
-    }
-    __syncthreads();
-#pragma unroll
-    for (int kk = 0; kk < 16; kk++) {
-      float a[4], b[4];
-#pragma unroll
-      for (int i=0;i<4;i++) a[i] = As[kk][ty*4+i];
-#pragma unroll
-      for (int j=0;j<4;j++) b[j] = Ws[kk][tx*4+j];
-#pragma unroll
-      for (int i=0;i<4;i++)
-#pragma unroll
-        for (int j=0;j<4;j++)
-          acc[i][j] += a[i]*b[j];
-    }
-    __syncthreads();
-  }
-  const float rscale = 1.f/sqrtf((float)K);
-  float a2 = 0.f, inv1a2 = 1.f;
-  if (FLAGS & F_RESID) { float al = alphap[0]; a2 = al*al; inv1a2 = 1.f/(1.f+a2); }
-#pragma unroll
-  for (int i=0;i<4;i++) {
-    int row = bm + ty*4 + i;
-    float ev = (FLAGS & F_ENV) ? env[row] : 1.f;
-#pragma unroll
-    for (int j=0;j<4;j++) {
-      int col = bn + tx*4 + j;
-      if (col >= N) continue;
-      float v = acc[i][j]*rscale;
-      if (FLAGS & F_SILU) v = v/(1.f+__expf(-v));
-      if (FLAGS & F_ENV)  v *= ev;
-      if (FLAGS & F_RESID) v = (Xres[(size_t)row*N+col] + a2*v)*inv1a2;
-      Cout[(size_t)row*N+col] = v;
-    }
-  }
 }
 
 __global__ __launch_bounds__(256) void dense16_k(const unsigned short* __restrict__ A,
@@ -741,35 +777,6 @@
   for (int k = 0; k < 256; k++)
     acc += As[(r<<8)+k] * W[(k<<4)+n];
   C[((size_t)(r0+r)<<4)+n] = acc * 0.0625f;
-}
-
-__global__ __launch_bounds__(256) void dense16v_k(const unsigned short* __restrict__ A,
-    const float* __restrict__ W0, const float* __restrict__ W1,
-    const float* __restrict__ Y, unsigned short* __restrict__ V,
-    float* __restrict__ wb)
-{
-  __shared__ float As[16*256];
-  __shared__ float w0s[256];
-  const int r0 = blockIdx.x << 4;
-  const int tid = threadIdx.x;
-  for (int i = tid; i < 16*256; i += 256)
-    As[i] = h2f(A[((size_t)r0<<8) + i]);
-  __syncthreads();
-  const int r = tid >> 4, n = tid & 15;
-  float a0 = 0.f, a1 = 0.f;
-#pragma unroll 8
-  for (int k = 0; k < 256; k++) {
-    float xv = As[(r<<8)+k];
-    a0 += xv * W0[(k<<4)+n];
-    a1 += xv * W1[(k<<4)+n];
-  }
-  w0s[tid] = a0 * 0.0625f;
-  wb[((size_t)(r0+r)<<4)+n] = a1 * 0.0625f;
-  __syncthreads();
-  for (int i = tid; i < 4096; i += 256) {
-    int e = i >> 8, idx = i & 255;
-    V[(((size_t)(r0+e))<<8) + idx] = f2h(w0s[(e<<4)+(idx&15)] * Y[((r0+e)<<4)+(idx>>4)]);
-  }
 }
 
 __global__ void edge_init_k(const float* __restrict__ vectors, const int* __restrict__ senders,
@@ -885,36 +892,6 @@
   tp0[((size_t)e<<6) + pmeta[p*4+0] + m] = f2h(acc * eps);
 }
 
-
-static void launch_gemm(int flags, const float* A1, const float* A2, int K1, int K,
-    const float* W, int N, float* C, const float* env, const float* alphap,
-    const float* Xres, hipStream_t stream)
-{
-  dim3 grid(E_EDGES/64, (N+63)/64);
-  switch(flags){
-    case F_SILU:        gemm_k<F_SILU>       <<<grid,256,0,stream>>>(A1,A2,K1,K,W,N,C,env,alphap,Xres); break;
-    case F_ENV:         gemm_k<F_ENV>        <<<grid,256,0,stream>>>(A1,A2,K1,K,W,N,C,env,alphap,Xres); break;
-    default: break;
-  }
-}
-
-static void launch_mgemm(int flags, int a16, const void* A1, const void* A2, int K1, int K,
-    const unsigned short* Wt, int N, unsigned short* C, const float* env,
-    const float* alphap, const unsigned short* Xres, hipStream_t stream)
-{
-  dim3 grid(E_EDGES/128, N/128);
-  if (a16) {
-    switch(flags){
-      case F_ENV:         mgemm_k<F_ENV,1>        <<<grid,256,0,stream>>>(A1,A2,K1,K,Wt,N,C,env,alphap,Xres); break;
-      default: break;
-    }
-  } else {
-    switch(flags){
-      case F_SILU:        mgemm_k<F_SILU,0>       <<<grid,256,0,stream>>>(A1,A2,K1,K,Wt,N,C,env,alphap,Xres); break;
-      default: break;
-    }
-  }
-}
 
 extern "C" void kernel_launch(void* const* d_in, const int* in_sizes, int n_in,
                               void* d_out, int out_size, void* d_ws, size_t ws_size,
@@ -965,8 +942,7 @@
   float* Yb    = (float*)alloc((size_t)E_EDGES*16*4);
   float* xb    = (float*)alloc((size_t)E_EDGES*256*4);
   float* Vb    = (float*)alloc((size_t)E_EDGES*256*4);
-  float* bufA  = (float*)alloc((size_t)E_EDGES*256*4);
-  float* bufB  = (float*)alloc((size_t)E_EDGES*256*4);
+  float* bufA  = (float*)alloc((size_t)E_EDGES*72*4);
   float* wb    = (float*)alloc((size_t)E_EDGES*16*4);
   float* tp0b  = (float*)alloc((size_t)E_EDGES*64*4);
   float* nodeb = (float*)alloc((size_t)NNODES*256*4);
@@ -976,8 +952,11 @@
   int* cursorb = (int*)alloc(NNODES*4);
   int* permb   = (int*)alloc(E_EDGES*4);
   unsigned short* Gt = (unsigned short*)alloc((size_t)256*Kdim*2);
-  unsigned short* Wt_tb3 = (unsigned short*)alloc(64*128*2);
-  unsigned short* Wt_tb4 = (unsigned short*)alloc(128*256*2);
+  unsigned short* Wt_tb1 = (unsigned short*)alloc(32*72*2);
+  unsigned short* Wt_tb2 = (unsigned short*)alloc(64*32*2);
+  unsigned short* Wt_tb3 = (unsigned short*)alloc(128*64*2);
+  unsigned short* Wt_tb4 = (unsigned short*)alloc(256*128*2);
+  unsigned short* Wt_w01 = (unsigned short*)alloc(32*256*2);
   unsigned short* Wt_l11 = (unsigned short*)alloc(320*256*2);
   unsigned short* Wt_l12 = (unsigned short*)alloc(256*256*2);
   unsigned short* Wt_l13 = (unsigned short*)alloc(256*256*2);
@@ -989,7 +968,6 @@
     return;
   }
   unsigned short* xb16 = (unsigned short*)xb;
-  unsigned short* bB16 = (unsigned short*)bufB;
   unsigned short* tp016 = (unsigned short*)tp0b;
   unsigned short* V16 = (unsigned short*)Vb;
 
@@ -1012,17 +990,20 @@
   }
   {
     WPack p;
-    p.d[0] = { W_tb3, Wt_tb3,  64, 7 };
-    p.d[1] = { W_tb4, Wt_tb4, 128, 8 };
-    p.d[2] = { W_l11, Wt_l11, 320, 8 };
-    p.d[3] = { W_l12, Wt_l12, 256, 8 };
-    p.d[4] = { W_l13, Wt_l13, 256, 8 };
-    p.d[5] = { W_l21, Wt_l21, 320, 8 };
-    p.d[6] = { W_l22, Wt_l22, 256, 8 };
-    p.d[7] = { W_l23, Wt_l23, 256, 8 };
-    dim3 g(320, 8);
+    p.d[0] = { W_tb1, Wt_tb1,  72, 5 };
+    p.d[1] = { W_tb2, Wt_tb2,  32, 6 };
+    p.d[2] = { W_tb3, Wt_tb3,  64, 7 };
+    p.d[3] = { W_tb4, Wt_tb4, 128, 8 };
+    p.d[4] = { W_l11, Wt_l11, 320, 8 };
+    p.d[5] = { W_l12, Wt_l12, 256, 8 };
+    p.d[6] = { W_l13, Wt_l13, 256, 8 };
+    p.d[7] = { W_l21, Wt_l21, 320, 8 };
+    p.d[8] = { W_l22, Wt_l22, 256, 8 };
+    p.d[9] = { W_l23, Wt_l23, 256, 8 };
+    dim3 g(320, 10);
     wcvt_k<<<g, 256, 0, stream>>>(p);
   }
+  wcvt01_k<<<32, 256, 0, stream>>>(W_w0, W_w1, Wt_w01);
   whc_k<<<1, 256, 0, stream>>>(W_h, W_out, hcb);
 
   hipMemsetAsync(cntb, 0, NNODES*4, stream);
@@ -1032,11 +1013,8 @@
 
   edge_init_k<<<E_EDGES/256, 256, 0, stream>>>(vectors, senders, receivers, species,
                                                emb, envb, Yb, bufA);
-  launch_gemm (F_SILU, bufA, nullptr, 72, 72,  W_tb1, 32,  bufB, envb, alpha, nullptr, stream);
-  launch_gemm (F_SILU, bufB, nullptr, 32, 32,  W_tb2, 64,  bufA, envb, alpha, nullptr, stream);
-  launch_mgemm(F_SILU, 0, bufA, nullptr, 64, 64,  Wt_tb3, 128, bB16, envb, alpha, nullptr, stream);
-  launch_mgemm(F_ENV,  1, bB16, nullptr, 128,128, Wt_tb4, 256, xb16, envb, alpha, nullptr, stream);
-  dense16v_k<<<E_EDGES/16, 256, 0, stream>>>(xb16, W_w0, W_w1, Yb, V16, wb);
+  tb_fused_k<<<E_EDGES/64, 256, 0, stream>>>(bufA, Wt_tb1, Wt_tb2, Wt_tb3, Wt_tb4,
+                                             Wt_w01, Yb, envb, xb16, V16, wb);
 
   nodesum_k<<<NNODES, 256, 0, stream>>>(wb, Yb, permb, startsb, nodeb);
   vn_k<<<E_EDGES/VN_E, 512, 0, stream>>>(nodeb, V16, senders, vareps, t_pr, Gt,
```

New measurement: 405.0 us (median of 2 runs). 7.2% less time.
